# Performance work log

Measured on AMD Instinct MI355X. Metric: run time of the kernel, lower is better.

The kernel has to match this reference:

```python
import jax, jax.numpy as jnp
import numpy as np

DIM_IN = 1024
DIM_OUT = 1024
NUM_HEADS = 16
HEAD_DIM = DIM_OUT // NUM_HEADS


def setup_inputs() -> dict:
    key = jax.random.key(0)
    k1, k2, k3, k4 = jax.random.split(key, 4)
    X = jax.random.normal(k1, (4, 2048, DIM_IN), dtype=jnp.float32)
    W_qkv = jax.random.normal(k2, (DIM_IN, 3 * DIM_OUT), dtype=jnp.float32) * (DIM_IN ** -0.5)
    W_out = jax.random.normal(k3, (DIM_OUT, DIM_OUT), dtype=jnp.float32) * (DIM_OUT ** -0.5)
    b_out = jax.random.normal(k4, (DIM_OUT,), dtype=jnp.float32) * 0.01
    return {"X": X, "W_qkv": W_qkv, "W_out": W_out, "b_out": b_out}


def reference(X, W_qkv, W_out, b_out):
    B, S, _ = X.shape
    qkv = X @ W_qkv  # [B, S, 3*dim_out]
    qkv = qkv.reshape(B, S, 3, NUM_HEADS, HEAD_DIM).transpose(2, 0, 3, 1, 4)
    q, k, v = qkv[0], qkv[1], qkv[2]  # each [B, H, S, hd]
    scores = jnp.einsum('bhqd,bhkd->bhqk', q, k)  # [B, H, S, S]
    causal = jnp.triu(jnp.ones((S, S), dtype=bool), k=1)
    scores = jnp.where(causal, -jnp.inf, scores)
    attn = jax.nn.softmax(scores * (HEAD_DIM ** -0.5), axis=-1)
    ctx = jnp.einsum('bhqk,bhkd->bhqd', attn, v)  # [B, H, S, hd]
    ctx = ctx.transpose(0, 2, 1, 3).reshape(B, S, DIM_OUT)
    return ctx @ W_out + b_out
```

## Files before the change

### kernel.cpp

```cpp
#include <hip/hip_runtime.h>
#include <hip/hip_bf16.h>

typedef __bf16 bf16_t;
typedef __bf16 bf16x8 __attribute__((ext_vector_type(8)));
typedef __bf16 bf16x4 __attribute__((ext_vector_type(4)));
typedef float f32x4 __attribute__((ext_vector_type(4)));

#define AS1(p) ((const __attribute__((address_space(1))) void*)(p))
#define AS3(p) ((__attribute__((address_space(3))) void*)(p))

#define QSCALE 0.1803368801111204f

__global__ void cast_x_kernel(const float* __restrict__ X, bf16_t* __restrict__ Xb) {
  int i = (blockIdx.x * 256 + threadIdx.x) * 4;
  float4 v = *(const float4*)(X + i);
  bf16x4 o;
  o[0] = (bf16_t)v.x; o[1] = (bf16_t)v.y; o[2] = (bf16_t)v.z; o[3] = (bf16_t)v.w;
  *(bf16x4*)(Xb + i) = o;
}

__global__ void transpose_cast_kernel(const float* __restrict__ W, bf16_t* __restrict__ Wt,
                                      int K, int N) {
  __shared__ float tile[32][33];
  int n0 = blockIdx.x * 32, k0 = blockIdx.y * 32;
  int tx = threadIdx.x, ty = threadIdx.y;
  for (int r = ty; r < 32; r += 8)
    tile[r][tx] = W[(size_t)(k0 + r) * N + n0 + tx];
  __syncthreads();
  for (int r = ty; r < 32; r += 8)
    Wt[(size_t)(n0 + r) * K + k0 + tx] = (bf16_t)tile[tx][r];
}

__global__ __launch_bounds__(256) void gemm_qkv_kernel(
    const bf16_t* __restrict__ A, const bf16_t* __restrict__ Bt,
    bf16_t* __restrict__ Qb, bf16_t* __restrict__ Kb, bf16_t* __restrict__ Vt) {
  __shared__ __align__(16) bf16_t As[128 * 32];
  __shared__ __align__(16) bf16_t Bs[128 * 32];
  const int tid = threadIdx.x;
  const int lane = tid & 63, wave = tid >> 6;
  const int quad = lane >> 4, l15 = lane & 15;
  const int wr = wave >> 1, wc = wave & 1;
  const int m0 = blockIdx.x * 128, n0 = blockIdx.y * 128;
  f32x4 acc[4][4];
  const f32x4 vzero = {0.f, 0.f, 0.f, 0.f};
#pragma unroll
  for (int i = 0; i < 4; i++)
#pragma unroll
    for (int j = 0; j < 4; j++) acc[i][j] = vzero;

  for (int kb = 0; kb < 1024; kb += 32) {
    __syncthreads();
#pragma unroll
    for (int i = 0; i < 2; i++) {
      int c = i * 256 + tid;
      int row = c >> 2, kc = c & 3;
      __builtin_amdgcn_global_load_lds(AS1(A + (size_t)(m0 + row) * 1024 + kb + kc * 8),
                                       AS3(As + c * 8), 16, 0, 0);
    }
#pragma unroll
    for (int i = 0; i < 2; i++) {
      int c = i * 256 + tid;
      int row = c >> 2, kc = c & 3;
      __builtin_amdgcn_global_load_lds(AS1(Bt + (size_t)(n0 + row) * 1024 + kb + kc * 8),
                                       AS3(Bs + c * 8), 16, 0, 0);
    }
    __builtin_amdgcn_s_waitcnt(0);
    __syncthreads();
    bf16x8 af[4], bfr[4];
#pragma unroll
    for (int t = 0; t < 4; t++) {
      af[t]  = *(const bf16x8*)(As + (wr * 64 + t * 16 + l15) * 32 + quad * 8);
      bfr[t] = *(const bf16x8*)(Bs + (wc * 64 + t * 16 + l15) * 32 + quad * 8);
    }
#pragma unroll
    for (int mt = 0; mt < 4; mt++)
#pragma unroll
      for (int nt = 0; nt < 4; nt++)
        acc[mt][nt] = __builtin_amdgcn_mfma_f32_16x16x32_bf16(af[mt], bfr[nt], acc[mt][nt], 0, 0, 0);
  }
#pragma unroll
  for (int nt = 0; nt < 4; nt++) {
    int gn = n0 + wc * 64 + nt * 16 + l15;
    int which = gn >> 10;
    int rem = gn & 1023;
    int hh = rem >> 6, dd = rem & 63;
    if (which == 2) {
#pragma unroll
      for (int mt = 0; mt < 4; mt++) {
        int gm0 = m0 + wr * 64 + mt * 16 + quad * 4;
        int b = gm0 >> 11, s = gm0 & 2047;
        bf16x4 o;
#pragma unroll
        for (int r = 0; r < 4; r++) o[r] = (bf16_t)acc[mt][nt][r];
        *(bf16x4*)(Vt + ((size_t)((b << 4) + hh) * 64 + dd) * 2048 + s) = o;
      }
    } else {
      bf16_t* dst = (which == 0) ? Qb : Kb;
      float scl = (which == 0) ? QSCALE : 1.0f;
#pragma unroll
      for (int mt = 0; mt < 4; mt++) {
#pragma unroll
        for (int r = 0; r < 4; r++) {
          int gm = m0 + wr * 64 + mt * 16 + quad * 4 + r;
          int b = gm >> 11, s = gm & 2047;
          dst[((size_t)((b << 4) + hh) * 2048 + s) * 64 + dd] = (bf16_t)(acc[mt][nt][r] * scl);
        }
      }
    }
  }
}

__global__ __launch_bounds__(256, 3) void attn_kernel(
    const bf16_t* __restrict__ Qg_, const bf16_t* __restrict__ Kg_,
    const bf16_t* __restrict__ Vtg_, bf16_t* __restrict__ ctx) {
  __shared__ __align__(16) bf16_t Ks[128 * 72];
  __shared__ __align__(16) bf16_t Vst[64 * 136];
  const int tid = threadIdx.x;
  const int lane = tid & 63, w = tid >> 6;
  const int quad = lane >> 4, l15 = lane & 15;

  const int bh = blockIdx.x >> 3;
  const int pp = blockIdx.x & 7;
  const int b = bh >> 4, h = bh & 15;
  const size_t base = (size_t)bh * 2048 * 64;
  const bf16_t* Kg = Kg_ + base;
  const bf16_t* Vtg = Vtg_ + base;

  bf16x8 kr[4], vr[4];
#pragma unroll
  for (int i = 0; i < 4; i++) {
    int c = i * 256 + tid;
    int r = c >> 3, dc = c & 7;
    kr[i] = *(const bf16x8*)(Kg + (size_t)r * 64 + dc * 8);
  }
#pragma unroll
  for (int i = 0; i < 4; i++) {
    int c = i * 256 + tid;
    int r = c >> 4, cc = c & 15;
    vr[i] = *(const bf16x8*)(Vtg + (size_t)r * 2048 + cc * 8);
  }

  const f32x4 vzero = {0.f, 0.f, 0.f, 0.f};

  for (int ti = 0; ti < 2; ti++) {
    const int qb = (ti == 0) ? pp : 15 - pp;
    const int L = qb + 1;

    bf16x8 aq[2][2];
#pragma unroll
    for (int mt = 0; mt < 2; mt++)
#pragma unroll
      for (int ks = 0; ks < 2; ks++)
        aq[mt][ks] = *(const bf16x8*)(Qg_ + base +
                                      (size_t)(qb * 128 + w * 32 + mt * 16 + l15) * 64 +
                                      ks * 32 + quad * 8);

    f32x4 Oacc[2][4];
    float rsum[2];
#pragma unroll
    for (int mt = 0; mt < 2; mt++) {
#pragma unroll
      for (int dt = 0; dt < 4; dt++) Oacc[mt][dt] = vzero;
      rsum[mt] = 0.f;
    }

    for (int j = 0; j < L; j++) {
      __syncthreads();
#pragma unroll
      for (int i = 0; i < 4; i++) {
        int c = i * 256 + tid;
        int k = c >> 3, dc = c & 7;
        int kp = (k & 0x60) | ((k & 4) << 2) | ((k & 0x18) >> 1) | (k & 3);
        *(bf16x8*)(Ks + kp * 72 + dc * 8) = kr[i];
      }
#pragma unroll
      for (int i = 0; i < 4; i++) {
        int c = i * 256 + tid;
        int r = c >> 4, cc = c & 15;
        *(bf16x8*)(Vst + r * 136 + cc * 8) = vr[i];
      }
      __syncthreads();

      const bool havenext = (j + 1 < L) || (ti == 0);
      if (havenext) {
        const int jn = (j + 1 < L) ? j + 1 : 0;
#pragma unroll
        for (int i = 0; i < 4; i++) {
          int c = i * 256 + tid;
          int r = c >> 3, dc = c & 7;
          kr[i] = *(const bf16x8*)(Kg + ((size_t)jn * 128 + r) * 64 + dc * 8);
        }
#pragma unroll
        for (int i = 0; i < 4; i++) {
          int c = i * 256 + tid;
          int r = c >> 4, cc = c & 15;
          vr[i] = *(const bf16x8*)(Vtg + (size_t)r * 2048 + jn * 128 + cc * 8);
        }
      }

      const bool diag = (j == L - 1);

#pragma unroll
      for (int g = 0; g < 4; g++) {
        f32x4 sch[2][2];
#pragma unroll
        for (int bs = 0; bs < 2; bs++) {
          const int nt = 2 * g + bs;
          bf16x8 bk0 = *(const bf16x8*)(Ks + (nt * 16 + l15) * 72 + quad * 8);
          bf16x8 bk1 = *(const bf16x8*)(Ks + (nt * 16 + l15) * 72 + 32 + quad * 8);
#pragma unroll
          for (int mt = 0; mt < 2; mt++) {
            f32x4 s0 = __builtin_amdgcn_mfma_f32_16x16x32_bf16(bk0, aq[mt][0], vzero, 0, 0, 0);
            sch[bs][mt] = __builtin_amdgcn_mfma_f32_16x16x32_bf16(bk1, aq[mt][1], s0, 0, 0, 0);
          }
        }
        bf16x8 pfrag[2];
#pragma unroll
        for (int mt = 0; mt < 2; mt++) {
          const int qg_ = qb * 128 + w * 32 + mt * 16 + l15;
#pragma unroll
          for (int bs = 0; bs < 2; bs++) {
            const int kb_ = j * 128 + g * 32 + quad * 8 + bs * 4;
#pragma unroll
            for (int r = 0; r < 4; r++) {
              float x = sch[bs][mt][r];
              if (diag && (kb_ + r > qg_)) x = -INFINITY;
              float p = __builtin_exp2f(x);
              rsum[mt] += p;
              pfrag[mt][bs * 4 + r] = (bf16_t)p;
            }
          }
        }
#pragma unroll
        for (int dt = 0; dt < 4; dt++) {
          bf16x8 bv = *(const bf16x8*)(Vst + (dt * 16 + l15) * 136 + g * 32 + quad * 8);
#pragma unroll
          for (int mt = 0; mt < 2; mt++)
            Oacc[mt][dt] = __builtin_amdgcn_mfma_f32_16x16x32_bf16(pfrag[mt], bv, Oacc[mt][dt], 0, 0, 0);
        }
      }
    }

#pragma unroll
    for (int mt = 0; mt < 2; mt++) {
      float s = rsum[mt];
      s += __shfl_xor(s, 16);
      s += __shfl_xor(s, 32);
      float rl[4];
#pragma unroll
      for (int r = 0; r < 4; r++)
        rl[r] = __builtin_amdgcn_rcpf(__shfl(s, quad * 4 + r));
#pragma unroll
      for (int dt = 0; dt < 4; dt++)
#pragma unroll
        for (int r = 0; r < 4; r++) {
          int qg = qb * 128 + w * 32 + mt * 16 + quad * 4 + r;
          ctx[((size_t)b * 2048 + qg) * 1024 + h * 64 + dt * 16 + l15] =
              (bf16_t)(Oacc[mt][dt][r] * rl[r]);
        }
    }
  }
}

__global__ __launch_bounds__(256) void gemm_out_kernel(
    const bf16_t* __restrict__ A, const bf16_t* __restrict__ Bt,
    const float* __restrict__ bias, float* __restrict__ out) {
  __shared__ __align__(16) bf16_t As[128 * 32];
  __shared__ __align__(16) bf16_t Bs[128 * 32];
  const int tid = threadIdx.x;
  const int lane = tid & 63, wave = tid >> 6;
  const int quad = lane >> 4, l15 = lane & 15;
  const int wr = wave >> 1, wc = wave & 1;
  const int m0 = blockIdx.x * 128, n0 = blockIdx.y * 128;
  f32x4 acc[4][4];
  const f32x4 vzero = {0.f, 0.f, 0.f, 0.f};
#pragma unroll
  for (int i = 0; i < 4; i++)
#pragma unroll
    for (int j = 0; j < 4; j++) acc[i][j] = vzero;

  for (int kb = 0; kb < 1024; kb += 32) {
    __syncthreads();
#pragma unroll
    for (int i = 0; i < 2; i++) {
      int c = i * 256 + tid;
      int row = c >> 2, kc = c & 3;
      __builtin_amdgcn_global_load_lds(AS1(A + (size_t)(m0 + row) * 1024 + kb + kc * 8),
                                       AS3(As + c * 8), 16, 0, 0);
    }
#pragma unroll
    for (int i = 0; i < 2; i++) {
      int c = i * 256 + tid;
      int row = c >> 2, kc = c & 3;
      __builtin_amdgcn_global_load_lds(AS1(Bt + (size_t)(n0 + row) * 1024 + kb + kc * 8),
                                       AS3(Bs + c * 8), 16, 0, 0);
    }
    __builtin_amdgcn_s_waitcnt(0);
    __syncthreads();
    bf16x8 af[4], bfr[4];
#pragma unroll
    for (int t = 0; t < 4; t++) {
      af[t]  = *(const bf16x8*)(As + (wr * 64 + t * 16 + l15) * 32 + quad * 8);
      bfr[t] = *(const bf16x8*)(Bs + (wc * 64 + t * 16 + l15) * 32 + quad * 8);
    }
#pragma unroll
    for (int mt = 0; mt < 4; mt++)
#pragma unroll
      for (int nt = 0; nt < 4; nt++)
        acc[mt][nt] = __builtin_amdgcn_mfma_f32_16x16x32_bf16(af[mt], bfr[nt], acc[mt][nt], 0, 0, 0);
  }
#pragma unroll
  for (int nt = 0; nt < 4; nt++) {
    int gn = n0 + wc * 64 + nt * 16 + l15;
    float bv = bias[gn];
#pragma unroll
    for (int mt = 0; mt < 4; mt++) {
#pragma unroll
      for (int r = 0; r < 4; r++) {
        int gm = m0 + wr * 64 + mt * 16 + quad * 4 + r;
        out[(size_t)gm * 1024 + gn] = acc[mt][nt][r] + bv;
      }
    }
  }
}

extern "C" void kernel_launch(void* const* d_in, const int* in_sizes, int n_in,
                              void* d_out, int out_size, void* d_ws, size_t ws_size,
                              hipStream_t stream) {
  (void)in_sizes; (void)n_in; (void)out_size; (void)ws_size;
  const float* X     = (const float*)d_in[0];
  const float* W_qkv = (const float*)d_in[1];
  const float* W_out = (const float*)d_in[2];
  const float* b_out = (const float*)d_in[3];
  float* out = (float*)d_out;

  char* ws = (char*)d_ws;
  bf16_t* Xb    = (bf16_t*)(ws);
  bf16_t* Wqkvt = (bf16_t*)(ws + 16777216);
  bf16_t* Woutt = (bf16_t*)(ws + 23068672);
  bf16_t* Qb    = (bf16_t*)(ws + 25165824);
  bf16_t* Kb    = (bf16_t*)(ws + 41943040);
  bf16_t* Vt    = (bf16_t*)(ws + 58720256);
  bf16_t* ctx   = (bf16_t*)(ws + 75497472);

  cast_x_kernel<<<8192, 256, 0, stream>>>(X, Xb);
  transpose_cast_kernel<<<dim3(96, 32), dim3(32, 8), 0, stream>>>(W_qkv, Wqkvt, 1024, 3072);
  transpose_cast_kernel<<<dim3(32, 32), dim3(32, 8), 0, stream>>>(W_out, Woutt, 1024, 1024);
  gemm_qkv_kernel<<<dim3(64, 24), 256, 0, stream>>>(Xb, Wqkvt, Qb, Kb, Vt);
  attn_kernel<<<dim3(512), 256, 0, stream>>>(Qb, Kb, Vt, ctx);
  gemm_out_kernel<<<dim3(64, 8), 256, 0, stream>>>(ctx, Woutt, b_out, out);
}
```

Measured before the change: 274.7 us.

## Halve attention query tile to 64 rows and double grid size

Attention blocks now process 64-row query tiles (16 rows per wave) instead of 128, with 32 query blocks per head, paired as bx and 31-bx to balance the causal work. The grid doubles to 1024 blocks and launch bounds ask for 4 blocks per SM, aiming for better occupancy and finer load balance. In exchange, each K/V tile loaded into shared memory is reused by half as many query rows, which doubles K/V global and LDS traffic, and the causal diagonal block wastes more masked compute.

New measurement: 295.3 us. 1.08x slower.

```diff
diff --git a/kernel.cpp b/kernel.cpp
--- a/kernel.cpp
+++ b/kernel.cpp
@@ -110,7 +110,7 @@
   }
 }
 
-__global__ __launch_bounds__(256, 3) void attn_kernel(
+__global__ __launch_bounds__(256, 4) void attn_kernel(
     const bf16_t* __restrict__ Qg_, const bf16_t* __restrict__ Kg_,
     const bf16_t* __restrict__ Vtg_, bf16_t* __restrict__ ctx) {
   __shared__ __align__(16) bf16_t Ks[128 * 72];
@@ -119,8 +119,8 @@
   const int lane = tid & 63, w = tid >> 6;
   const int quad = lane >> 4, l15 = lane & 15;
 
-  const int bh = blockIdx.x >> 3;
-  const int pp = blockIdx.x & 7;
+  const int bh = blockIdx.x >> 4;
+  const int bx = blockIdx.x & 15;
   const int b = bh >> 4, h = bh & 15;
   const size_t base = (size_t)bh * 2048 * 64;
   const bf16_t* Kg = Kg_ + base;
@@ -143,26 +143,20 @@
   const f32x4 vzero = {0.f, 0.f, 0.f, 0.f};
 
   for (int ti = 0; ti < 2; ti++) {
-    const int qb = (ti == 0) ? pp : 15 - pp;
-    const int L = qb + 1;
-
-    bf16x8 aq[2][2];
-#pragma unroll
-    for (int mt = 0; mt < 2; mt++)
-#pragma unroll
-      for (int ks = 0; ks < 2; ks++)
-        aq[mt][ks] = *(const bf16x8*)(Qg_ + base +
-                                      (size_t)(qb * 128 + w * 32 + mt * 16 + l15) * 64 +
-                                      ks * 32 + quad * 8);
-
-    f32x4 Oacc[2][4];
-    float rsum[2];
-#pragma unroll
-    for (int mt = 0; mt < 2; mt++) {
-#pragma unroll
-      for (int dt = 0; dt < 4; dt++) Oacc[mt][dt] = vzero;
-      rsum[mt] = 0.f;
-    }
+    const int qb = (ti == 0) ? bx : 31 - bx;
+    const int L = (qb >> 1) + 1;
+
+    bf16x8 aq[2];
+#pragma unroll
+    for (int ks = 0; ks < 2; ks++)
+      aq[ks] = *(const bf16x8*)(Qg_ + base +
+                                (size_t)(qb * 64 + w * 16 + l15) * 64 +
+                                ks * 32 + quad * 8);
+
+    f32x4 Oacc[4];
+    float rsum = 0.f;
+#pragma unroll
+    for (int dt = 0; dt < 4; dt++) Oacc[dt] = vzero;
 
     for (int j = 0; j < L; j++) {
       __syncthreads();
@@ -202,48 +196,39 @@
 
 #pragma unroll
       for (int g = 0; g < 4; g++) {
-        f32x4 sch[2][2];
+        f32x4 sch[2];
 #pragma unroll
         for (int bs = 0; bs < 2; bs++) {
           const int nt = 2 * g + bs;
           bf16x8 bk0 = *(const bf16x8*)(Ks + (nt * 16 + l15) * 72 + quad * 8);
           bf16x8 bk1 = *(const bf16x8*)(Ks + (nt * 16 + l15) * 72 + 32 + quad * 8);
-#pragma unroll
-          for (int mt = 0; mt < 2; mt++) {
-            f32x4 s0 = __builtin_amdgcn_mfma_f32_16x16x32_bf16(bk0, aq[mt][0], vzero, 0, 0, 0);
-            sch[bs][mt] = __builtin_amdgcn_mfma_f32_16x16x32_bf16(bk1, aq[mt][1], s0, 0, 0, 0);
-          }
-        }
-        bf16x8 pfrag[2];
-#pragma unroll
-        for (int mt = 0; mt < 2; mt++) {
-          const int qg_ = qb * 128 + w * 32 + mt * 16 + l15;
-#pragma unroll
-          for (int bs = 0; bs < 2; bs++) {
-            const int kb_ = j * 128 + g * 32 + quad * 8 + bs * 4;
-#pragma unroll
-            for (int r = 0; r < 4; r++) {
-              float x = sch[bs][mt][r];
-              if (diag && (kb_ + r > qg_)) x = -INFINITY;
-              float p = __builtin_exp2f(x);
-              rsum[mt] += p;
-              pfrag[mt][bs * 4 + r] = (bf16_t)p;
-            }
+          f32x4 s0 = __builtin_amdgcn_mfma_f32_16x16x32_bf16(bk0, aq[0], vzero, 0, 0, 0);
+          sch[bs] = __builtin_amdgcn_mfma_f32_16x16x32_bf16(bk1, aq[1], s0, 0, 0, 0);
+        }
+        bf16x8 pfrag;
+        const int qg_ = qb * 64 + w * 16 + l15;
+#pragma unroll
+        for (int bs = 0; bs < 2; bs++) {
+          const int kb_ = j * 128 + g * 32 + quad * 8 + bs * 4;
+#pragma unroll
+          for (int r = 0; r < 4; r++) {
+            float x = sch[bs][r];
+            if (diag && (kb_ + r > qg_)) x = -INFINITY;
+            float p = __builtin_exp2f(x);
+            rsum += p;
+            pfrag[bs * 4 + r] = (bf16_t)p;
           }
         }
 #pragma unroll
         for (int dt = 0; dt < 4; dt++) {
           bf16x8 bv = *(const bf16x8*)(Vst + (dt * 16 + l15) * 136 + g * 32 + quad * 8);
-#pragma unroll
-          for (int mt = 0; mt < 2; mt++)
-            Oacc[mt][dt] = __builtin_amdgcn_mfma_f32_16x16x32_bf16(pfrag[mt], bv, Oacc[mt][dt], 0, 0, 0);
-        }
-      }
-    }
-
-#pragma unroll
-    for (int mt = 0; mt < 2; mt++) {
-      float s = rsum[mt];
+          Oacc[dt] = __builtin_amdgcn_mfma_f32_16x16x32_bf16(pfrag, bv, Oacc[dt], 0, 0, 0);
+        }
+      }
+    }
+
+    {
+      float s = rsum;
       s += __shfl_xor(s, 16);
       s += __shfl_xor(s, 32);
       float rl[4];
@@ -254,9 +239,9 @@
       for (int dt = 0; dt < 4; dt++)
 #pragma unroll
         for (int r = 0; r < 4; r++) {
-          int qg = qb * 128 + w * 32 + mt * 16 + quad * 4 + r;
+          int qg = qb * 64 + w * 16 + quad * 4 + r;
           ctx[((size_t)b * 2048 + qg) * 1024 + h * 64 + dt * 16 + l15] =
-              (bf16_t)(Oacc[mt][dt][r] * rl[r]);
+              (bf16_t)(Oacc[dt][r] * rl[r]);
         }
     }
   }
@@ -347,6 +332,6 @@
   transpose_cast_kernel<<<dim3(96, 32), dim3(32, 8), 0, stream>>>(W_qkv, Wqkvt, 1024, 3072);
   transpose_cast_kernel<<<dim3(32, 32), dim3(32, 8), 0, stream>>>(W_out, Woutt, 1024, 1024);
   gemm_qkv_kernel<<<dim3(64, 24), 256, 0, stream>>>(Xb, Wqkvt, Qb, Kb, Vt);
-  attn_kernel<<<dim3(512), 256, 0, stream>>>(Qb, Kb, Vt, ctx);
+  attn_kernel<<<dim3(1024), 256, 0, stream>>>(Qb, Kb, Vt, ctx);
   gemm_out_kernel<<<dim3(64, 8), 256, 0, stream>>>(ctx, Woutt, b_out, out);
 }
```
